# Optimization experiments

Measured on AMD Instinct MI355X. Metric: run time of the kernel, lower is better.

The kernel has to match this reference:

```python
import jax, jax.numpy as jnp
import numpy as np

B, D, CTX, H = 8192, 64, 256, 512  # batch, latent dim (made.nin), context dim, MADE hidden


def _masks(D, H):
    """Standard MADE natural-ordering masks (Germain et al. 2015)."""
    m0 = np.arange(1, D + 1)                 # input degrees 1..D
    mh = (np.arange(H) % (D - 1)) + 1        # hidden degrees 1..D-1
    M1 = (mh[:, None] >= m0[None, :]).astype(np.float32)   # (H, D)
    M2 = (mh[:, None] >= mh[None, :]).astype(np.float32)   # (H, H)
    mo = np.concatenate([m0, m0])            # outputs = [means; pre_scales]
    Mo = (mo[:, None] > mh[None, :]).astype(np.float32)    # (2D, H)
    return jnp.asarray(M1), jnp.asarray(M2), jnp.asarray(Mo)


def setup_inputs() -> dict:
    key = jax.random.key(0)
    ks = jax.random.split(key, 7)
    s = 0.05
    return {
        "context": jax.random.normal(ks[0], (B, CTX), jnp.float32),
        "eps": jax.random.normal(ks[1], (B, D), jnp.float32),  # reparameterization noise
        "W1": jax.random.normal(ks[2], (H, D), jnp.float32) * s,
        "b1": jnp.zeros((H,), jnp.float32),
        "Wc": jax.random.normal(ks[3], (H, CTX), jnp.float32) * s,
        "W2": jax.random.normal(ks[4], (H, H), jnp.float32) * s,
        "b2": jnp.zeros((H,), jnp.float32),
        "Wo": jax.random.normal(ks[5], (2 * D, H), jnp.float32) * s,
        "bo": jnp.zeros((2 * D,), jnp.float32),
    }


def reference(context, eps, W1, b1, Wc, W2, b2, Wo, bo):
    """AutoRegressiveDistribution.rsample (gaussian): D sequential MADE forwards,
    each extracting column i of (mu, softplus(pre_scale)) and sampling z_i."""
    M1, M2, Mo = _masks(D, H)
    W1m, W2m, Wom = (W1 * M1).T, (W2 * M2).T, (Wo * Mo).T
    ctx_h = context @ Wc.T  # context projection is constant across steps

    def step(z, i):
        h = jax.nn.relu(z @ W1m + ctx_h + b1)   # (B, H)
        h = jax.nn.relu(h @ W2m + b2)           # (B, H)
        out = h @ Wom + bo                      # (B, 2D): [means | pre_scales]
        mu_i = out[:, i]
        scale_i = jax.nn.softplus(out[:, D + i])
        z_i = mu_i + scale_i * eps[:, i]        # Normal(mu, scale).rsample()
        z = z.at[:, i].set(z_i)
        return z, (mu_i, scale_i)

    z0 = jnp.zeros((context.shape[0], D), context.dtype)
    z, (mus, scales) = jax.lax.scan(step, z0, jnp.arange(D))
    # state = (z_sample, mu_inferred, scale_inferred), each (B, D)
    return z, mus.T, scales.T
```

## Files before the change

### kernel.cpp

```cpp
#include <hip/hip_runtime.h>
#include <math.h>


typedef float f2 __attribute__((ext_vector_type(2)));

#define Bn 8192
#define Dn 64
#define CTXn 256
#define Hn 512
#define Rn 16
#define BD (Bn * Dn)

#define WQ_SZ  (64 * 512 * 12)
#define WOQ_SZ (64 * 64 * 20)
#define WCP_SZ (CTXn * Hn)
#define W1P_SZ (64 * 512)

#define BARRIER() do {                                      \
    asm volatile("s_waitcnt lgkmcnt(0)" ::: "memory");      \
    __builtin_amdgcn_s_barrier();                           \
    asm volatile("" ::: "memory");                          \
  } while (0)

#define WAVE_FENCE() asm volatile("s_waitcnt lgkmcnt(0)" ::: "memory")

__device__ __forceinline__ int perm_of(int p, int* degout) {
  int k, t;
  if (p < 72) { k = p / 9 + 1; t = p - (k - 1) * 9; }
  else        { int pp = p - 72; k = pp / 8 + 9; t = pp - (k - 9) * 8; }
  *degout = k;
  return (k - 1) + 63 * t;
}
__device__ __forceinline__ int inv_perm(int h) {
  int i = h % 63;
  int t = h / 63;
  int base = (i < 9) ? 9 * i : 72 + 8 * (i - 8);
  return base + t;
}

#define R0e 262144
#define R1e (R0e + 32768)
#define R2e (R1e + 65536)
#define R3e (R2e + 131072)
#define R4e (R3e + 35840)
#define R5e (R4e + 1024)
#define R6e (R5e + 32768)
__global__ void prep_kernel(const float* __restrict__ W1, const float* __restrict__ Wc,
                            const float* __restrict__ W2, const float* __restrict__ Wo,
                            const float* __restrict__ b1, const float* __restrict__ b2,
                            float* __restrict__ Wq, float* __restrict__ Woq,
                            float* __restrict__ WcpT, float* __restrict__ b1p,
                            float* __restrict__ b2p, float* __restrict__ W1p) {
  int idx = blockIdx.x * 256 + threadIdx.x;
  if (idx < R0e) {
    int hq = idx >> 9, hp = idx & 511;
    int i = hp % 63, e = hp / 63;
    Wq[i * 6144 + inv_perm(hq) * 12 + e] = W2[idx];
  } else if (idx < R1e) {
    int jj = idx - R0e;
    int hq = jj >> 6, i = jj & 63;
    Wq[i * 6144 + inv_perm(hq) * 12 + 9] = W1[jj];
  } else if (idx < R2e) {
    int jj = idx - R1e;
    int o = jj >> 9, hp = jj & 511;
    int i = hp % 63, p = hp / 63;
    int j = o & 63, half = o >> 6;
    Woq[i * 1280 + j * 20 + half * 10 + p] = Wo[jj];
  } else if (idx < R3e) {
    int jj = idx - R2e;
    int hq = jj >> 8, cc = jj & 255;
    int p = inv_perm(hq);
    int slot = (p < 256) ? (2 * p) : (2 * (p - 256) + 1);
    WcpT[cc * 512 + slot] = Wc[jj];
  } else if (idx < R4e) {
    int z = idx - R3e;
    if (z < 28672) {
      int i = 8 + (z >> 9), q = z & 511;
      Wq[i * 6144 + q * 12 + 8] = 0.f;
    } else {
      int z2 = z - 28672;
      int i = 8 + (z2 >> 7), r = z2 & 127;
      int j = r & 63, half = r >> 6;
      Woq[i * 1280 + j * 20 + half * 10 + 8] = 0.f;
    }
  } else if (idx < R5e) {
    int z = idx - R4e;
    if (z < 512) {
      int dq; int hq = perm_of(z, &dq);
      b1p[z] = b1[hq];
    } else {
      int q = z - 512;
      int dq; int hq = perm_of(q, &dq);
      b2p[q] = b2[hq];
    }
  } else if (idx < R6e) {
    int jj = idx - R5e;
    int hq = jj >> 6, i = jj & 63;
    W1p[i * 512 + inv_perm(hq)] = W1[jj];
  }
}

__global__ __launch_bounds__(256, 2)
void made_wp_kernel(
    const float* __restrict__ context, const float* __restrict__ WcpT,
    const float* __restrict__ b1p, const float* __restrict__ Wq,
    const float* __restrict__ Woq, const float* __restrict__ W1p,
    const float* __restrict__ b2p, const float* __restrict__ bo,
    const float* __restrict__ eps, float* __restrict__ out) {
  __shared__ __align__(16) float ctxR[Rn][264];
  __shared__ __align__(16) float a1x[512][17];
  __shared__ __align__(16) float zpub[4][4];
  __shared__ __align__(16) float h1pub[4][9][4];
  __shared__ __align__(16) float h2pub[4][9][4];

  int t = threadIdx.x;
  int w = t >> 6, lane = t & 63;
  int b0 = blockIdx.x * Rn;
  int r0 = b0 + 4 * w;

  #pragma unroll
  for (int r = 0; r < Rn; ++r)
    ctxR[r][t] = context[(b0 + r) * CTXn + t];
  BARRIER();

  f2 accu[16];
  {
    f2 bias = (f2){b1p[t], b1p[t + 256]};
    #pragma unroll
    for (int r = 0; r < 16; ++r) accu[r] = bias;
  }
  {
    const float* wc = WcpT + 2 * t;
    #pragma clang loop unroll(disable)
    for (int c4 = 0; c4 < CTXn / 4; ++c4) {
      f2 wv0 = *(const f2*)&wc[0];
      f2 wv1 = *(const f2*)&wc[Hn];
      f2 wv2 = *(const f2*)&wc[2 * Hn];
      f2 wv3 = *(const f2*)&wc[3 * Hn];
      wc += 4 * Hn;
      #pragma unroll
      for (int hf = 0; hf < 2; ++hf) {
        float4 x[8];
        #pragma unroll
        for (int r = 0; r < 8; ++r) x[r] = *(const float4*)&ctxR[8 * hf + r][4 * c4];
        #pragma unroll
        for (int r = 0; r < 8; ++r) {
          accu[8 * hf + r] += (f2){x[r].x, x[r].x} * wv0;
          accu[8 * hf + r] += (f2){x[r].y, x[r].y} * wv1;
          accu[8 * hf + r] += (f2){x[r].z, x[r].z} * wv2;
          accu[8 * hf + r] += (f2){x[r].w, x[r].w} * wv3;
        }
      }
    }
  }

  #pragma unroll
  for (int r = 0; r < 16; ++r) {
    a1x[t][r] = accu[r].x;
    a1x[t + 256][r] = accu[r].y;
  }
  BARRIER();

  f2 a1[8][2];
  #pragma unroll
  for (int k = 0; k < 8; ++k) {
    int q = lane + 64 * k;
    a1[k][0] = (f2){a1x[q][4 * w + 0], a1x[q][4 * w + 1]};
    a1[k][1] = (f2){a1x[q][4 * w + 2], a1x[q][4 * w + 3]};
  }

  f2 a2[8][2];
  #pragma unroll
  for (int k = 0; k < 8; ++k) {
    float b = b2p[lane + 64 * k];
    a2[k][0] = (f2){b, b};
    a2[k][1] = (f2){b, b};
  }
  f2 ocA[2], ocB[2];
  {
    float ba = bo[lane], bb = bo[lane + 64];
    ocA[0] = ocA[1] = (f2){ba, ba};
    ocB[0] = ocB[1] = (f2){bb, bb};
  }
  f2 ez[2];
  ez[0] = (f2){eps[(r0 + 0) * Dn + lane], eps[(r0 + 1) * Dn + lane]};
  ez[1] = (f2){eps[(r0 + 2) * Dn + lane], eps[(r0 + 3) * Dn + lane]};

  #pragma clang loop unroll(disable)
  for (int S = 0; S < Dn; ++S) {
    bool fin = (S <= 62);

    float4 wqv[8][3];
    float w1v[8];
    if (fin) {
      const float* wbase = Wq + (size_t)S * 6144;
      const float* w1base = W1p + (size_t)S * 512;
      #pragma unroll
      for (int k = 0; k < 8; ++k) {
        const float4* pq = (const float4*)(wbase + (size_t)(lane + 64 * k) * 12);
        wqv[k][0] = pq[0]; wqv[k][1] = pq[1]; wqv[k][2] = pq[2];
        w1v[k] = w1base[lane + 64 * k];
      }
    }

    if (lane == S) {
      f2 zv0, zv1;
      #pragma unroll
      for (int rr = 0; rr < 2; ++rr) {
        f2 pre = ocB[rr];
        float sx = fmaxf(pre.x, 0.f) + __logf(1.f + __expf(-fabsf(pre.x)));
        float sy = fmaxf(pre.y, 0.f) + __logf(1.f + __expf(-fabsf(pre.y)));
        f2 sc = (f2){sx, sy};
        f2 z = ocA[rr] + sc * ez[rr];
        out[(r0 + 2 * rr) * Dn + S] = z.x;
        out[(r0 + 2 * rr + 1) * Dn + S] = z.y;
        out[BD + (r0 + 2 * rr) * Dn + S] = ocA[rr].x;
        out[BD + (r0 + 2 * rr + 1) * Dn + S] = ocA[rr].y;
        out[2 * BD + (r0 + 2 * rr) * Dn + S] = sc.x;
        out[2 * BD + (r0 + 2 * rr + 1) * Dn + S] = sc.y;
        if (rr == 0) zv0 = z; else zv1 = z;
      }
      *(float4*)&zpub[w][0] = (float4){zv0.x, zv0.y, zv1.x, zv1.y};
    }
    WAVE_FENCE();

    if (fin) {
      int sb = (S < 8) ? 9 * S : 8 * S + 8;
      int e = (S < 8) ? 9 : 8;
      int jj = (lane - sb) & 63;
      bool own = (jj < e);
      int qown = sb + jj;

      float4 zq = *(const float4*)&zpub[w][0];
      f2 zz0 = (f2){zq.x, zq.y}, zz1 = (f2){zq.z, zq.w};
      #pragma unroll
      for (int k = 0; k < 8; ++k) {
        f2 ww = (f2){w1v[k], w1v[k]};
        a1[k][0] += ww * zz0;
        a1[k][1] += ww * zz1;
      }
      const float4* wo = (const float4*)(Woq + (size_t)S * 1280 + (size_t)lane * 20);
      float4 wo0 = wo[0], wo1 = wo[1], wo2 = wo[2], wo3 = wo[3], wo4 = wo[4];

      if (own) {
        #pragma unroll
        for (int k = 0; k < 8; ++k) {
          if ((qown >> 6) == k) {
            *(float4*)&h1pub[w][jj][0] =
                (float4){fmaxf(a1[k][0].x, 0.f), fmaxf(a1[k][0].y, 0.f),
                         fmaxf(a1[k][1].x, 0.f), fmaxf(a1[k][1].y, 0.f)};
          }
        }
      }
      WAVE_FENCE();

      #pragma unroll
      for (int p = 0; p < 9; ++p) {
        float4 hv = *(const float4*)&h1pub[w][p][0];
        f2 h01 = (f2){hv.x, hv.y}, h23 = (f2){hv.z, hv.w};
        #pragma unroll
        for (int k = 0; k < 8; ++k) {
          float wsc = (p == 0) ? wqv[k][0].x : (p == 1) ? wqv[k][0].y
                    : (p == 2) ? wqv[k][0].z : (p == 3) ? wqv[k][0].w
                    : (p == 4) ? wqv[k][1].x : (p == 5) ? wqv[k][1].y
                    : (p == 6) ? wqv[k][1].z : (p == 7) ? wqv[k][1].w
                               : wqv[k][2].x;
          f2 ww = (f2){wsc, wsc};
          a2[k][0] += ww * h01;
          a2[k][1] += ww * h23;
        }
      }
      if (own) {
        #pragma unroll
        for (int k = 0; k < 8; ++k) {
          if ((qown >> 6) == k) {
            *(float4*)&h2pub[w][jj][0] =
                (float4){fmaxf(a2[k][0].x, 0.f), fmaxf(a2[k][0].y, 0.f),
                         fmaxf(a2[k][1].x, 0.f), fmaxf(a2[k][1].y, 0.f)};
          }
        }
      }
      WAVE_FENCE();

      {
        float wa[9] = {wo0.x, wo0.y, wo0.z, wo0.w, wo1.x, wo1.y, wo1.z, wo1.w, wo2.x};
        float wb[9] = {wo2.z, wo2.w, wo3.x, wo3.y, wo3.z, wo3.w, wo4.x, wo4.y, wo4.z};
        #pragma unroll
        for (int p = 0; p < 9; ++p) {
          float4 hv = *(const float4*)&h2pub[w][p][0];
          f2 h01 = (f2){hv.x, hv.y}, h23 = (f2){hv.z, hv.w};
          f2 va = (f2){wa[p], wa[p]}, vb = (f2){wb[p], wb[p]};
          ocA[0] += va * h01; ocA[1] += va * h23;
          ocB[0] += vb * h01; ocB[1] += vb * h23;
        }
      }
    }
  }
}

extern "C" void kernel_launch(void* const* d_in, const int* in_sizes, int n_in,
                              void* d_out, int out_size, void* d_ws, size_t ws_size,
                              hipStream_t stream) {
  const float* context = (const float*)d_in[0];
  const float* eps     = (const float*)d_in[1];
  const float* W1      = (const float*)d_in[2];
  const float* b1      = (const float*)d_in[3];
  const float* Wc      = (const float*)d_in[4];
  const float* W2      = (const float*)d_in[5];
  const float* b2      = (const float*)d_in[6];
  const float* Wo      = (const float*)d_in[7];
  const float* bo      = (const float*)d_in[8];
  float* out = (float*)d_out;

  float* ws   = (float*)d_ws;
  float* Wq   = ws;
  float* Woq  = Wq + WQ_SZ;
  float* WcpT = Woq + WOQ_SZ;
  float* b1p  = WcpT + WCP_SZ;
  float* b2p  = b1p + 512;
  float* W1p  = b2p + 512;

  prep_kernel<<<(R6e + 255) / 256, 256, 0, stream>>>(
      W1, Wc, W2, Wo, b1, b2, Wq, Woq, WcpT, b1p, b2p, W1p);
  made_wp_kernel<<<Bn / Rn, 256, 0, stream>>>(context, WcpT, b1p, Wq, Woq,
                                              W1p, b2p, bo, eps, out);
}
```

Baseline: 291.6 us.

## Repartition MADE work: hidden units across threads, 32 rows per block with block barriers

Doubles rows per block to 32 and reassigns work so each thread owns 4 hidden units across 16 rows, instead of each wave owning 4 rows across all 512 hidden units. Per-step weight loads are shared by more rows, which cuts the per-row weight traffic from Wq. The context projection now writes straight into register accumulators with a row-major Wc layout, removing the a1x LDS transpose and the separate W1p array (W1 is read from slot 9 of Wq). In exchange, each of the 64 steps needs three block-wide barriers instead of wave-local fences, occupancy drops to one block per launch-bounds setting, and there are half as many blocks (256).

```diff
diff --git a/kernel.cpp b/kernel.cpp
--- a/kernel.cpp
+++ b/kernel.cpp
@@ -8,21 +8,18 @@
 #define Dn 64
 #define CTXn 256
 #define Hn 512
-#define Rn 16
+#define Rn 32
 #define BD (Bn * Dn)
 
 #define WQ_SZ  (64 * 512 * 12)
 #define WOQ_SZ (64 * 64 * 20)
-#define WCP_SZ (CTXn * Hn)
-#define W1P_SZ (64 * 512)
+#define WCT_SZ (512 * 256)
 
 #define BARRIER() do {                                      \
     asm volatile("s_waitcnt lgkmcnt(0)" ::: "memory");      \
     __builtin_amdgcn_s_barrier();                           \
     asm volatile("" ::: "memory");                          \
   } while (0)
-
-#define WAVE_FENCE() asm volatile("s_waitcnt lgkmcnt(0)" ::: "memory")
 
 __device__ __forceinline__ int perm_of(int p, int* degout) {
   int k, t;
@@ -44,13 +41,12 @@
 #define R3e (R2e + 131072)
 #define R4e (R3e + 35840)
 #define R5e (R4e + 1024)
-#define R6e (R5e + 32768)
 __global__ void prep_kernel(const float* __restrict__ W1, const float* __restrict__ Wc,
                             const float* __restrict__ W2, const float* __restrict__ Wo,
                             const float* __restrict__ b1, const float* __restrict__ b2,
                             float* __restrict__ Wq, float* __restrict__ Woq,
-                            float* __restrict__ WcpT, float* __restrict__ b1p,
-                            float* __restrict__ b2p, float* __restrict__ W1p) {
+                            float* __restrict__ WcT2, float* __restrict__ b1p,
+                            float* __restrict__ b2p) {
   int idx = blockIdx.x * 256 + threadIdx.x;
   if (idx < R0e) {
     int hq = idx >> 9, hp = idx & 511;
@@ -69,9 +65,7 @@
   } else if (idx < R3e) {
     int jj = idx - R2e;
     int hq = jj >> 8, cc = jj & 255;
-    int p = inv_perm(hq);
-    int slot = (p < 256) ? (2 * p) : (2 * (p - 256) + 1);
-    WcpT[cc * 512 + slot] = Wc[jj];
+    WcT2[inv_perm(hq) * 256 + cc] = Wc[jj];
   } else if (idx < R4e) {
     int z = idx - R3e;
     if (z < 28672) {
@@ -93,206 +87,222 @@
       int dq; int hq = perm_of(q, &dq);
       b2p[q] = b2[hq];
     }
-  } else if (idx < R6e) {
-    int jj = idx - R5e;
-    int hq = jj >> 6, i = jj & 63;
-    W1p[i * 512 + inv_perm(hq)] = W1[jj];
-  }
-}
-
-__global__ __launch_bounds__(256, 2)
-void made_wp_kernel(
-    const float* __restrict__ context, const float* __restrict__ WcpT,
+  }
+}
+
+__global__ __launch_bounds__(256, 1)
+void made_v22_kernel(
+    const float* __restrict__ context, const float* __restrict__ WcT2,
     const float* __restrict__ b1p, const float* __restrict__ Wq,
-    const float* __restrict__ Woq, const float* __restrict__ W1p,
-    const float* __restrict__ b2p, const float* __restrict__ bo,
-    const float* __restrict__ eps, float* __restrict__ out) {
+    const float* __restrict__ Woq, const float* __restrict__ b2p,
+    const float* __restrict__ bo, const float* __restrict__ eps,
+    float* __restrict__ out) {
   __shared__ __align__(16) float ctxR[Rn][264];
-  __shared__ __align__(16) float a1x[512][17];
-  __shared__ __align__(16) float zpub[4][4];
-  __shared__ __align__(16) float h1pub[4][9][4];
-  __shared__ __align__(16) float h2pub[4][9][4];
+  __shared__ __align__(16) float zcur[32];
+  __shared__ __align__(16) float h1g[9][32];
+  __shared__ __align__(16) float h2g[9][32];
 
   int t = threadIdx.x;
-  int w = t >> 6, lane = t & 63;
+  int w = t >> 6, l = t & 63;
+  int rh = t >> 7, tq = t & 127;
   int b0 = blockIdx.x * Rn;
-  int r0 = b0 + 4 * w;
+  int fr = 16 * rh;
+  int dr0 = b0 + 8 * w;
+
+  int qk[4], gk[4];
+  #pragma unroll
+  for (int k = 0; k < 4; ++k) {
+    qk[k] = tq + 128 * k;
+    gk[k] = (qk[k] < 72) ? qk[k] / 9 : (qk[k] - 72) / 8 + 8;
+  }
 
   #pragma unroll
   for (int r = 0; r < Rn; ++r)
     ctxR[r][t] = context[(b0 + r) * CTXn + t];
   BARRIER();
 
-  f2 accu[16];
+  f2 a1[4][8];
+  #pragma unroll
+  for (int k = 0; k < 4; ++k) {
+    float b = b1p[qk[k]];
+    #pragma unroll
+    for (int rr = 0; rr < 8; ++rr) a1[k][rr] = (f2){b, b};
+  }
   {
-    f2 bias = (f2){b1p[t], b1p[t + 256]};
+    #pragma clang loop unroll(disable)
+    for (int c4 = 0; c4 < 64; ++c4) {
+      float4 xr[16];
+      #pragma unroll
+      for (int r = 0; r < 16; ++r)
+        xr[r] = *(const float4*)&ctxR[fr + r][4 * c4];
+      float4 wv[4];
+      #pragma unroll
+      for (int k = 0; k < 4; ++k)
+        wv[k] = *(const float4*)&WcT2[(size_t)qk[k] * 256 + 4 * c4];
+      #pragma unroll
+      for (int cc = 0; cc < 4; ++cc) {
+        f2 x[8];
+        #pragma unroll
+        for (int rr = 0; rr < 8; ++rr) {
+          float xa = (cc == 0) ? xr[2 * rr].x : (cc == 1) ? xr[2 * rr].y
+                   : (cc == 2) ? xr[2 * rr].z : xr[2 * rr].w;
+          float xb = (cc == 0) ? xr[2 * rr + 1].x : (cc == 1) ? xr[2 * rr + 1].y
+                   : (cc == 2) ? xr[2 * rr + 1].z : xr[2 * rr + 1].w;
+          x[rr] = (f2){xa, xb};
+        }
+        #pragma unroll
+        for (int k = 0; k < 4; ++k) {
+          float ws = (cc == 0) ? wv[k].x : (cc == 1) ? wv[k].y
+                   : (cc == 2) ? wv[k].z : wv[k].w;
+          f2 ww = (f2){ws, ws};
+          #pragma unroll
+          for (int rr = 0; rr < 8; ++rr) a1[k][rr] += ww * x[rr];
+        }
+      }
+    }
+  }
+
+  f2 a2[4][8];
+  #pragma unroll
+  for (int k = 0; k < 4; ++k) {
+    float b = b2p[qk[k]];
     #pragma unroll
-    for (int r = 0; r < 16; ++r) accu[r] = bias;
-  }
+    for (int rr = 0; rr < 8; ++rr) a2[k][rr] = (f2){b, b};
+  }
+  f2 ocA[4], ocB[4];
   {
-    const float* wc = WcpT + 2 * t;
-    #pragma clang loop unroll(disable)
-    for (int c4 = 0; c4 < CTXn / 4; ++c4) {
-      f2 wv0 = *(const f2*)&wc[0];
-      f2 wv1 = *(const f2*)&wc[Hn];
-      f2 wv2 = *(const f2*)&wc[2 * Hn];
-      f2 wv3 = *(const f2*)&wc[3 * Hn];
-      wc += 4 * Hn;
-      #pragma unroll
-      for (int hf = 0; hf < 2; ++hf) {
-        float4 x[8];
-        #pragma unroll
-        for (int r = 0; r < 8; ++r) x[r] = *(const float4*)&ctxR[8 * hf + r][4 * c4];
-        #pragma unroll
-        for (int r = 0; r < 8; ++r) {
-          accu[8 * hf + r] += (f2){x[r].x, x[r].x} * wv0;
-          accu[8 * hf + r] += (f2){x[r].y, x[r].y} * wv1;
-          accu[8 * hf + r] += (f2){x[r].z, x[r].z} * wv2;
-          accu[8 * hf + r] += (f2){x[r].w, x[r].w} * wv3;
-        }
-      }
-    }
-  }
-
-  #pragma unroll
-  for (int r = 0; r < 16; ++r) {
-    a1x[t][r] = accu[r].x;
-    a1x[t + 256][r] = accu[r].y;
-  }
-  BARRIER();
-
-  f2 a1[8][2];
-  #pragma unroll
-  for (int k = 0; k < 8; ++k) {
-    int q = lane + 64 * k;
-    a1[k][0] = (f2){a1x[q][4 * w + 0], a1x[q][4 * w + 1]};
-    a1[k][1] = (f2){a1x[q][4 * w + 2], a1x[q][4 * w + 3]};
-  }
-
-  f2 a2[8][2];
-  #pragma unroll
-  for (int k = 0; k < 8; ++k) {
-    float b = b2p[lane + 64 * k];
-    a2[k][0] = (f2){b, b};
-    a2[k][1] = (f2){b, b};
-  }
-  f2 ocA[2], ocB[2];
-  {
-    float ba = bo[lane], bb = bo[lane + 64];
-    ocA[0] = ocA[1] = (f2){ba, ba};
-    ocB[0] = ocB[1] = (f2){bb, bb};
-  }
-  f2 ez[2];
-  ez[0] = (f2){eps[(r0 + 0) * Dn + lane], eps[(r0 + 1) * Dn + lane]};
-  ez[1] = (f2){eps[(r0 + 2) * Dn + lane], eps[(r0 + 3) * Dn + lane]};
+    float ba = bo[l], bb = bo[l + 64];
+    #pragma unroll
+    for (int jj = 0; jj < 4; ++jj) { ocA[jj] = (f2){ba, ba}; ocB[jj] = (f2){bb, bb}; }
+  }
+  f2 ez[4];
+  #pragma unroll
+  for (int jj = 0; jj < 4; ++jj)
+    ez[jj] = (f2){eps[(dr0 + 2 * jj) * Dn + l], eps[(dr0 + 2 * jj + 1) * Dn + l]};
 
   #pragma clang loop unroll(disable)
-  for (int S = 0; S < Dn; ++S) {
-    bool fin = (S <= 62);
-
-    float4 wqv[8][3];
-    float w1v[8];
-    if (fin) {
-      const float* wbase = Wq + (size_t)S * 6144;
-      const float* w1base = W1p + (size_t)S * 512;
-      #pragma unroll
-      for (int k = 0; k < 8; ++k) {
-        const float4* pq = (const float4*)(wbase + (size_t)(lane + 64 * k) * 12);
-        wqv[k][0] = pq[0]; wqv[k][1] = pq[1]; wqv[k][2] = pq[2];
-        w1v[k] = w1base[lane + 64 * k];
-      }
-    }
-
-    if (lane == S) {
-      f2 zv0, zv1;
-      #pragma unroll
-      for (int rr = 0; rr < 2; ++rr) {
-        f2 pre = ocB[rr];
+  for (int i = 0; i < Dn; ++i) {
+    bool fin = (i < 63);
+
+    if (l == i) {
+      float4 zq0, zq1;
+      #pragma unroll
+      for (int jj = 0; jj < 4; ++jj) {
+        f2 pre = ocB[jj];
         float sx = fmaxf(pre.x, 0.f) + __logf(1.f + __expf(-fabsf(pre.x)));
         float sy = fmaxf(pre.y, 0.f) + __logf(1.f + __expf(-fabsf(pre.y)));
         f2 sc = (f2){sx, sy};
-        f2 z = ocA[rr] + sc * ez[rr];
-        out[(r0 + 2 * rr) * Dn + S] = z.x;
-        out[(r0 + 2 * rr + 1) * Dn + S] = z.y;
-        out[BD + (r0 + 2 * rr) * Dn + S] = ocA[rr].x;
-        out[BD + (r0 + 2 * rr + 1) * Dn + S] = ocA[rr].y;
-        out[2 * BD + (r0 + 2 * rr) * Dn + S] = sc.x;
-        out[2 * BD + (r0 + 2 * rr + 1) * Dn + S] = sc.y;
-        if (rr == 0) zv0 = z; else zv1 = z;
-      }
-      *(float4*)&zpub[w][0] = (float4){zv0.x, zv0.y, zv1.x, zv1.y};
-    }
-    WAVE_FENCE();
-
+        f2 z = ocA[jj] + sc * ez[jj];
+        out[(dr0 + 2 * jj) * Dn + i] = z.x;
+        out[(dr0 + 2 * jj + 1) * Dn + i] = z.y;
+        out[BD + (dr0 + 2 * jj) * Dn + i] = ocA[jj].x;
+        out[BD + (dr0 + 2 * jj + 1) * Dn + i] = ocA[jj].y;
+        out[2 * BD + (dr0 + 2 * jj) * Dn + i] = sc.x;
+        out[2 * BD + (dr0 + 2 * jj + 1) * Dn + i] = sc.y;
+        if (jj == 0) { zq0.x = z.x; zq0.y = z.y; }
+        if (jj == 1) { zq0.z = z.x; zq0.w = z.y; }
+        if (jj == 2) { zq1.x = z.x; zq1.y = z.y; }
+        if (jj == 3) { zq1.z = z.x; zq1.w = z.y; }
+      }
+      *(float4*)&zcur[8 * w] = zq0;
+      *(float4*)&zcur[8 * w + 4] = zq1;
+    }
+    BARRIER();
+
+    int sb = (i < 8) ? 9 * i : 8 * i + 8;
+    float4 wq[4][3];
     if (fin) {
-      int sb = (S < 8) ? 9 * S : 8 * S + 8;
-      int e = (S < 8) ? 9 : 8;
-      int jj = (lane - sb) & 63;
-      bool own = (jj < e);
-      int qown = sb + jj;
-
-      float4 zq = *(const float4*)&zpub[w][0];
-      f2 zz0 = (f2){zq.x, zq.y}, zz1 = (f2){zq.z, zq.w};
-      #pragma unroll
-      for (int k = 0; k < 8; ++k) {
-        f2 ww = (f2){w1v[k], w1v[k]};
-        a1[k][0] += ww * zz0;
-        a1[k][1] += ww * zz1;
-      }
-      const float4* wo = (const float4*)(Woq + (size_t)S * 1280 + (size_t)lane * 20);
-      float4 wo0 = wo[0], wo1 = wo[1], wo2 = wo[2], wo3 = wo[3], wo4 = wo[4];
-
-      if (own) {
+      #pragma unroll
+      for (int k = 0; k < 4; ++k) {
+        const float4* pq =
+            (const float4*)(Wq + (size_t)i * 6144 + (size_t)qk[k] * 12);
+        wq[k][0] = pq[0]; wq[k][1] = pq[1]; wq[k][2] = pq[2];
+      }
+      float4 z0 = *(const float4*)&zcur[fr];
+      float4 z1 = *(const float4*)&zcur[fr + 4];
+      float4 z2 = *(const float4*)&zcur[fr + 8];
+      float4 z3 = *(const float4*)&zcur[fr + 12];
+      f2 zz[8] = {(f2){z0.x, z0.y}, (f2){z0.z, z0.w},
+                  (f2){z1.x, z1.y}, (f2){z1.z, z1.w},
+                  (f2){z2.x, z2.y}, (f2){z2.z, z2.w},
+                  (f2){z3.x, z3.y}, (f2){z3.z, z3.w}};
+      #pragma unroll
+      for (int k = 0; k < 4; ++k) {
+        f2 ww = (f2){wq[k][2].y, wq[k][2].y};
         #pragma unroll
-        for (int k = 0; k < 8; ++k) {
-          if ((qown >> 6) == k) {
-            *(float4*)&h1pub[w][jj][0] =
-                (float4){fmaxf(a1[k][0].x, 0.f), fmaxf(a1[k][0].y, 0.f),
-                         fmaxf(a1[k][1].x, 0.f), fmaxf(a1[k][1].y, 0.f)};
+        for (int rr = 0; rr < 8; ++rr) a1[k][rr] += ww * zz[rr];
+      }
+      #pragma unroll
+      for (int k = 0; k < 4; ++k) {
+        if (gk[k] == i) {
+          int pp = qk[k] - sb;
+          #pragma unroll
+          for (int s = 0; s < 4; ++s) {
+            float4 h = {fmaxf(a1[k][2 * s].x, 0.f), fmaxf(a1[k][2 * s].y, 0.f),
+                        fmaxf(a1[k][2 * s + 1].x, 0.f), fmaxf(a1[k][2 * s + 1].y, 0.f)};
+            *(float4*)&h1g[pp][fr + 4 * s] = h;
           }
         }
       }
-      WAVE_FENCE();
+    }
+    BARRIER();
+
+    float4 wo0, wo1, wo2, wo3, wo4;
+    if (fin) {
+      const float4* wo = (const float4*)(Woq + (size_t)i * 1280 + (size_t)l * 20);
+      wo0 = wo[0]; wo1 = wo[1]; wo2 = wo[2]; wo3 = wo[3]; wo4 = wo[4];
 
       #pragma unroll
       for (int p = 0; p < 9; ++p) {
-        float4 hv = *(const float4*)&h1pub[w][p][0];
-        f2 h01 = (f2){hv.x, hv.y}, h23 = (f2){hv.z, hv.w};
+        float4 ha = *(const float4*)&h1g[p][fr];
+        float4 hb = *(const float4*)&h1g[p][fr + 4];
+        float4 hc = *(const float4*)&h1g[p][fr + 8];
+        float4 hd = *(const float4*)&h1g[p][fr + 12];
+        f2 h[8] = {(f2){ha.x, ha.y}, (f2){ha.z, ha.w},
+                   (f2){hb.x, hb.y}, (f2){hb.z, hb.w},
+                   (f2){hc.x, hc.y}, (f2){hc.z, hc.w},
+                   (f2){hd.x, hd.y}, (f2){hd.z, hd.w}};
         #pragma unroll
-        for (int k = 0; k < 8; ++k) {
-          float wsc = (p == 0) ? wqv[k][0].x : (p == 1) ? wqv[k][0].y
-                    : (p == 2) ? wqv[k][0].z : (p == 3) ? wqv[k][0].w
-                    : (p == 4) ? wqv[k][1].x : (p == 5) ? wqv[k][1].y
-                    : (p == 6) ? wqv[k][1].z : (p == 7) ? wqv[k][1].w
-                               : wqv[k][2].x;
-          f2 ww = (f2){wsc, wsc};
-          a2[k][0] += ww * h01;
-          a2[k][1] += ww * h23;
-        }
-      }
-      if (own) {
-        #pragma unroll
-        for (int k = 0; k < 8; ++k) {
-          if ((qown >> 6) == k) {
-            *(float4*)&h2pub[w][jj][0] =
-                (float4){fmaxf(a2[k][0].x, 0.f), fmaxf(a2[k][0].y, 0.f),
-                         fmaxf(a2[k][1].x, 0.f), fmaxf(a2[k][1].y, 0.f)};
+        for (int k = 0; k < 4; ++k) {
+          float ws = (p == 0) ? wq[k][0].x : (p == 1) ? wq[k][0].y
+                   : (p == 2) ? wq[k][0].z : (p == 3) ? wq[k][0].w
+                   : (p == 4) ? wq[k][1].x : (p == 5) ? wq[k][1].y
+                   : (p == 6) ? wq[k][1].z : (p == 7) ? wq[k][1].w
+                              : wq[k][2].x;
+          f2 ww = (f2){ws, ws};
+          #pragma unroll
+          for (int rr = 0; rr < 8; ++rr) a2[k][rr] += ww * h[rr];
+        }
+      }
+      #pragma unroll
+      for (int k = 0; k < 4; ++k) {
+        if (gk[k] == i) {
+          int pp = qk[k] - sb;
+          #pragma unroll
+          for (int s = 0; s < 4; ++s) {
+            float4 h = {fmaxf(a2[k][2 * s].x, 0.f), fmaxf(a2[k][2 * s].y, 0.f),
+                        fmaxf(a2[k][2 * s + 1].x, 0.f), fmaxf(a2[k][2 * s + 1].y, 0.f)};
+            *(float4*)&h2g[pp][fr + 4 * s] = h;
           }
         }
       }
-      WAVE_FENCE();
-
-      {
-        float wa[9] = {wo0.x, wo0.y, wo0.z, wo0.w, wo1.x, wo1.y, wo1.z, wo1.w, wo2.x};
-        float wb[9] = {wo2.z, wo2.w, wo3.x, wo3.y, wo3.z, wo3.w, wo4.x, wo4.y, wo4.z};
-        #pragma unroll
-        for (int p = 0; p < 9; ++p) {
-          float4 hv = *(const float4*)&h2pub[w][p][0];
-          f2 h01 = (f2){hv.x, hv.y}, h23 = (f2){hv.z, hv.w};
-          f2 va = (f2){wa[p], wa[p]}, vb = (f2){wb[p], wb[p]};
-          ocA[0] += va * h01; ocA[1] += va * h23;
-          ocB[0] += vb * h01; ocB[1] += vb * h23;
-        }
+    }
+    BARRIER();
+
+    if (fin) {
+      float wa[9] = {wo0.x, wo0.y, wo0.z, wo0.w, wo1.x, wo1.y, wo1.z, wo1.w, wo2.x};
+      float wb[9] = {wo2.z, wo2.w, wo3.x, wo3.y, wo3.z, wo3.w, wo4.x, wo4.y, wo4.z};
+      #pragma unroll
+      for (int p = 0; p < 9; ++p) {
+        float4 h0 = *(const float4*)&h2g[p][8 * w];
+        float4 h1_ = *(const float4*)&h2g[p][8 * w + 4];
+        f2 ha = (f2){h0.x, h0.y}, hbp = (f2){h0.z, h0.w};
+        f2 hcp = (f2){h1_.x, h1_.y}, hdp = (f2){h1_.z, h1_.w};
+        f2 va = (f2){wa[p], wa[p]}, vb = (f2){wb[p], wb[p]};
+        ocA[0] += va * ha; ocA[1] += va * hbp;
+        ocA[2] += va * hcp; ocA[3] += va * hdp;
+        ocB[0] += vb * ha; ocB[1] += vb * hbp;
+        ocB[2] += vb * hcp; ocB[3] += vb * hdp;
       }
     }
   }
@@ -315,13 +325,12 @@
   float* ws   = (float*)d_ws;
   float* Wq   = ws;
   float* Woq  = Wq + WQ_SZ;
-  float* WcpT = Woq + WOQ_SZ;
-  float* b1p  = WcpT + WCP_SZ;
+  float* WcT2 = Woq + WOQ_SZ;
+  float* b1p  = WcT2 + WCT_SZ;
   float* b2p  = b1p + 512;
-  float* W1p  = b2p + 512;
-
-  prep_kernel<<<(R6e + 255) / 256, 256, 0, stream>>>(
-      W1, Wc, W2, Wo, b1, b2, Wq, Woq, WcpT, b1p, b2p, W1p);
-  made_wp_kernel<<<Bn / Rn, 256, 0, stream>>>(context, WcpT, b1p, Wq, Woq,
-                                              W1p, b2p, bo, eps, out);
-}
+
+  prep_kernel<<<(R5e + 255) / 256, 256, 0, stream>>>(
+      W1, Wc, W2, Wo, b1, b2, Wq, Woq, WcT2, b1p, b2p);
+  made_v22_kernel<<<Bn / Rn, 256, 0, stream>>>(context, WcT2, b1p, Wq, Woq,
+                                               b2p, bo, eps, out);
+}
```

After: 341.0 us. 17.0% more time.
